# Kernel tuning notes

Measured on AMD Instinct MI355X. Metric: run time of the kernel, lower is better.

Reference implementation:

```python
import jax, jax.numpy as jnp
import numpy as np
from jax import lax

B, T, C = 2, 2048, 2048
N_HEADS, N_KV_HEADS = 16, 1
HEAD_DIM = C // N_HEADS  # 128
ROPE_THETA = 10000.0


def setup_inputs() -> dict:
    key = jax.random.key(0)
    ks = jax.random.split(key, 8)
    x = jax.random.normal(ks[0], (B, T, C), dtype=jnp.float32)
    # rotary frequencies: freqs_cis = exp(1j * t * theta^{-2i/d}) -> cos/sin halves
    inv_freq = 1.0 / (ROPE_THETA ** (np.arange(0, HEAD_DIM, 2, dtype=np.float32) / HEAD_DIM))
    t = np.arange(T, dtype=np.float32)
    ang = np.outer(t, inv_freq)  # [T, HEAD_DIM//2]
    freqs_cos = jnp.asarray(np.cos(ang), dtype=jnp.float32)
    freqs_sin = jnp.asarray(np.sin(ang), dtype=jnp.float32)
    # additive causal mask [1,1,T,T]
    causal = jnp.tril(jnp.ones((T, T), dtype=bool))
    mask = jnp.where(causal, 0.0, -1e9).astype(jnp.float32)[None, None]
    s = 0.02
    wq_k = jax.random.normal(ks[1], (C, N_HEADS * HEAD_DIM), dtype=jnp.float32) * s
    wk_k = jax.random.normal(ks[2], (C, N_KV_HEADS * HEAD_DIM), dtype=jnp.float32) * s
    wv_k = jax.random.normal(ks[3], (C, N_KV_HEADS * HEAD_DIM), dtype=jnp.float32) * s
    wo_k = jax.random.normal(ks[4], (N_HEADS * HEAD_DIM, C), dtype=jnp.float32) * s
    return {
        "x": x, "freqs_cos": freqs_cos, "freqs_sin": freqs_sin, "mask": mask,
        "wq_k": wq_k, "wq_b": jnp.zeros((N_HEADS * HEAD_DIM,), jnp.float32),
        "wk_k": wk_k, "wk_b": jnp.zeros((N_KV_HEADS * HEAD_DIM,), jnp.float32),
        "wv_k": wv_k, "wv_b": jnp.zeros((N_KV_HEADS * HEAD_DIM,), jnp.float32),
        "wo_k": wo_k, "wo_b": jnp.zeros((C,), jnp.float32),
    }


def _rope(xq, xk, cos, sin):
    # xq: [B,T,H,D], xk: [B,T,Hkv,D]; cos/sin: [T, D//2]
    def rot(v):
        vr = v.reshape(*v.shape[:-1], -1, 2)  # [..., D//2, 2]
        re, im = vr[..., 0], vr[..., 1]
        c = cos[None, :, None, :]
        s = sin[None, :, None, :]
        out_re = re * c - im * s
        out_im = re * s + im * c
        return jnp.stack([out_re, out_im], axis=-1).reshape(v.shape)
    return rot(xq), rot(xk)


def reference(x, freqs_cos, freqs_sin, mask, wq_k, wq_b, wk_k, wk_b, wv_k, wv_b, wo_k, wo_b):
    b, t, c = x.shape
    head_dim = c // N_HEADS
    q = (x @ wq_k + wq_b).reshape(b, t, N_HEADS, head_dim)
    k = (x @ wk_k + wk_b).reshape(b, t, N_KV_HEADS, head_dim)
    v = (x @ wv_k + wv_b).reshape(b, t, N_KV_HEADS, head_dim)
    q, k = _rope(q, k, freqs_cos[:t], freqs_sin[:t])
    if N_HEADS > N_KV_HEADS:
        rep = N_HEADS // N_KV_HEADS
        k = jnp.repeat(k, rep, axis=2)
        v = jnp.repeat(v, rep, axis=2)
    q, k, v = (jnp.swapaxes(a, 1, 2) for a in (q, k, v))  # [B,H,T,D]
    scale = 1.0 / jnp.sqrt(jnp.asarray(head_dim, x.dtype))
    scores = jnp.einsum('bhid,bhjd->bhij', q, k) * scale + mask
    scores = scores - lax.stop_gradient(jnp.max(scores, axis=-1, keepdims=True))
    w = jnp.exp(scores)
    attn = w / jnp.sum(w, axis=-1, keepdims=True)
    out = jnp.einsum('bhij,bhjd->bhid', attn, v)
    out = jnp.swapaxes(out, 1, 2).reshape(b, t, -1)
    return out @ wo_k + wo_b
```

## Files before the change

### kernel.cpp

```cpp
#include <hip/hip_runtime.h>
#include <hip/hip_bf16.h>

typedef __bf16 bf16;
typedef __bf16 bf16x4 __attribute__((ext_vector_type(4)));
typedef __bf16 bf16x8 __attribute__((ext_vector_type(8)));
typedef float  f32x4  __attribute__((ext_vector_type(4)));

#define MFMA(a,b,c) __builtin_amdgcn_mfma_f32_16x16x32_bf16(a,b,c,0,0,0)

__device__ __forceinline__ void load_lds16(const void* gptr, void* lptr) {
  __builtin_amdgcn_global_load_lds(
      (const __attribute__((address_space(1))) void*)gptr,
      (__attribute__((address_space(3))) void*)lptr, 16, 0, 0);
}


__global__ void cvt_bf16(const float* __restrict__ in, bf16* __restrict__ out, int n4) {
  int i = blockIdx.x * blockDim.x + threadIdx.x;
  if (i >= n4) return;
  float4 v = ((const float4*)in)[i];
  bf16x4 o = { (bf16)v.x, (bf16)v.y, (bf16)v.z, (bf16)v.w };
  ((bf16x4*)out)[i] = o;
}

__global__ void transpose_w(const float* __restrict__ src, bf16* __restrict__ dst, int ncols) {
  __shared__ float tl[32][33];
  int n0 = blockIdx.x * 32, k0 = blockIdx.y * 32;
  int tx = threadIdx.x, ty = threadIdx.y;
  for (int i = 0; i < 4; ++i)
    tl[ty + i*8][tx] = src[(size_t)(k0 + ty + i*8) * ncols + n0 + tx];
  __syncthreads();
  for (int i = 0; i < 4; ++i)
    dst[(size_t)(n0 + ty + i*8) * 2048 + k0 + tx] = (bf16)tl[tx][ty + i*8];
}

__global__ void concat_bias(const float* __restrict__ qb, const float* __restrict__ kb,
                            const float* __restrict__ vb, float* __restrict__ o) {
  int i = blockIdx.x * 256 + threadIdx.x;
  if (i >= 2304) return;
  o[i] = (i < 2048) ? qb[i] : (i < 2176 ? kb[i - 2048] : vb[i - 2176]);
}


template<bool OUT_F32>
__global__ __launch_bounds__(256) void gemm_bt(
    const bf16* __restrict__ A, const bf16* __restrict__ Bt,
    void* __restrict__ Cout, const float* __restrict__ bias,
    int M, int N, int K)
{
  __shared__ char smem[32768];
  char* As = smem;
  char* Bs = smem + 16384;
  const int tid = threadIdx.x;
  const int w = tid >> 6, l = tid & 63;
  const int lg = l >> 4, ll = l & 15;
  const int n0 = blockIdx.x * 128, m0 = blockIdx.y * 128;
  const int wr = w >> 1, wc = w & 1;

  f32x4 acc[4][4];
  for (int i = 0; i < 4; ++i) for (int j = 0; j < 4; ++j) acc[i][j] = (f32x4){0.f,0.f,0.f,0.f};

  for (int k0 = 0; k0 < K; k0 += 64) {
    for (int t = 0; t < 4; ++t) {
      int seg = w*4 + t;
      int row = seg*8 + (l >> 3);
      int cb  = (l & 7) * 8;
      load_lds16(A  + (size_t)(m0 + row) * K + k0 + cb, As + seg*1024);
      load_lds16(Bt + (size_t)(n0 + row) * K + k0 + cb, Bs + seg*1024);
    }
    __syncthreads();
    for (int kc = 0; kc < 2; ++kc) {
      bf16x8 af[4], bfr[4];
      for (int ai = 0; ai < 4; ++ai)
        af[ai]  = *(const bf16x8*)(As + (wr*64 + ai*16 + ll)*128 + kc*64 + lg*16);
      for (int bj = 0; bj < 4; ++bj)
        bfr[bj] = *(const bf16x8*)(Bs + (wc*64 + bj*16 + ll)*128 + kc*64 + lg*16);
      for (int ai = 0; ai < 4; ++ai)
        for (int bj = 0; bj < 4; ++bj)
          acc[ai][bj] = MFMA(af[ai], bfr[bj], acc[ai][bj]);
    }
    __syncthreads();
  }

  for (int ai = 0; ai < 4; ++ai) {
    int row = m0 + wr*64 + ai*16 + lg*4;
    for (int bj = 0; bj < 4; ++bj) {
      int col = n0 + wc*64 + bj*16 + ll;
      float bv = bias[col];
      for (int r = 0; r < 4; ++r) {
        float v = acc[ai][bj][r] + bv;
        if constexpr (OUT_F32) ((float*)Cout)[(size_t)(row + r) * N + col] = v;
        else                   ((bf16*)Cout)[(size_t)(row + r) * N + col] = (bf16)v;
      }
    }
  }
}


__global__ void rope_q(bf16* __restrict__ qkv, const float* __restrict__ fc, const float* __restrict__ fs) {
  int idx = blockIdx.x * 256 + threadIdx.x;
  int d = idx & 63, h = (idx >> 6) & 15, bt = idx >> 10;
  int t = bt & 2047;
  bf16* p = qkv + (size_t)bt * 2304 + h * 128 + 2 * d;
  float re = (float)p[0], im = (float)p[1];
  float c = fc[t*64 + d], s = fs[t*64 + d];
  p[0] = (bf16)(re * c - im * s);
  p[1] = (bf16)(re * s + im * c);
}

__global__ void rope_k(bf16* __restrict__ qkv, const float* __restrict__ fc, const float* __restrict__ fs) {
  int idx = blockIdx.x * 256 + threadIdx.x;
  int d = idx & 63, bt = idx >> 6;
  int t = bt & 2047;
  bf16* p = qkv + (size_t)bt * 2304 + 2048 + 2 * d;
  float re = (float)p[0], im = (float)p[1];
  float c = fc[t*64 + d], s = fs[t*64 + d];
  p[0] = (bf16)(re * c - im * s);
  p[1] = (bf16)(re * s + im * c);
}

__global__ void transpose_v(const bf16* __restrict__ qkv, bf16* __restrict__ vt) {
  __shared__ bf16 tl[32][33];
  int t0 = blockIdx.x * 32, d0 = blockIdx.y * 32, b = blockIdx.z;
  int tx = threadIdx.x, ty = threadIdx.y;
  for (int i = 0; i < 4; ++i)
    tl[ty + i*8][tx] = qkv[(size_t)(b*2048 + t0 + ty + i*8) * 2304 + 2176 + d0 + tx];
  __syncthreads();
  for (int i = 0; i < 4; ++i)
    vt[(size_t)(b*128 + d0 + ty + i*8) * 2048 + t0 + tx] = tl[tx][ty + i*8];
}


__global__ __launch_bounds__(256) void attn_kernel(
    const bf16* __restrict__ qkv, const bf16* __restrict__ vt, bf16* __restrict__ aout)
{
  constexpr int T = 2048, NQKV = 2304, D = 128;
  const int tid = threadIdx.x;
  const int w = tid >> 6, l = tid & 63;
  const int lg = l >> 4, ll = l & 15;
  const int h  = blockIdx.y;
  const int b  = blockIdx.z;

  __shared__ char smem[16384 + 16384 + 8192];
  char* Ks = smem;
  char* Vs = smem + 16384;
  char* Ps = smem + 32768 + w*2048;

  const size_t qkvb = (size_t)b * T * NQKV;
  const float scale = 0.08838834764831845f;

  for (int half = 0; half < 2; ++half) {
    const int x  = half ? (31 - blockIdx.x) : blockIdx.x;
    const int q0 = x * 64;

    bf16x8 qf[4];
    {
      int row = q0 + w*16 + ll;
      const bf16* qrow = qkv + qkvb + (size_t)row * NQKV + h * D;
      for (int kc = 0; kc < 4; ++kc)
        qf[kc] = *(const bf16x8*)(qrow + kc*32 + lg*8);
    }

    f32x4 acc[8];
    for (int dt = 0; dt < 8; ++dt) acc[dt] = (f32x4){0.f,0.f,0.f,0.f};
    float mx[4], sm[4];
    for (int r = 0; r < 4; ++r) { mx[r] = -3e38f; sm[r] = 0.f; }

    for (int j0 = 0; j0 <= q0; j0 += 64) {
      for (int t = 0; t < 4; ++t) {
        int seg = w*4 + t;
        int row = seg*4 + (l >> 4);
        int gcol = (((l & 15) * 16) ^ ((row & 7) << 4)) >> 1;
        load_lds16(qkv + qkvb + (size_t)(j0 + row) * NQKV + 2048 + gcol, Ks + seg*1024);
      }
      for (int t = 0; t < 4; ++t) {
        int seg = w*4 + t;
        int row = seg*8 + (l >> 3);
        int gcol = (((l & 7) * 16) ^ ((row & 7) << 4)) >> 1;
        load_lds16(vt + (size_t)(b*D + row) * T + j0 + gcol, Vs + seg*1024);
      }
      __syncthreads();

      f32x4 sv[4];
      for (int jt = 0; jt < 4; ++jt) {
        int row = jt*16 + ll;
        f32x4 s = (f32x4){0.f,0.f,0.f,0.f};
        for (int kc = 0; kc < 4; ++kc) {
          bf16x8 kf = *(const bf16x8*)(Ks + row*256 + ((kc*64 + lg*16) ^ ((row & 7) << 4)));
          s = MFMA(qf[kc], kf, s);
        }
        sv[jt] = s;
      }

      if (j0 == q0) {
        for (int jt = 0; jt < 4; ++jt)
          for (int r = 0; r < 4; ++r) {
            int i = w*16 + lg*4 + r;
            int j = jt*16 + ll;
            float v = sv[jt][r] * scale;
            sv[jt][r] = (j <= i) ? v : -1e9f;
          }
      } else {
        for (int jt = 0; jt < 4; ++jt)
          for (int r = 0; r < 4; ++r)
            sv[jt][r] *= scale;
      }

      for (int r = 0; r < 4; ++r) {
        float tm = fmaxf(fmaxf(sv[0][r], sv[1][r]), fmaxf(sv[2][r], sv[3][r]));
        tm = fmaxf(tm, __shfl_xor(tm, 1));
        tm = fmaxf(tm, __shfl_xor(tm, 2));
        tm = fmaxf(tm, __shfl_xor(tm, 4));
        tm = fmaxf(tm, __shfl_xor(tm, 8));
        float mo = mx[r];
        float mn = fmaxf(mo, tm);
        mx[r] = mn;
        float fac = __expf(mo - mn);
        float ps = 0.f;
        for (int jt = 0; jt < 4; ++jt) {
          float p = __expf(sv[jt][r] - mn);
          sv[jt][r] = p;
          ps += p;
        }
        ps += __shfl_xor(ps, 1);
        ps += __shfl_xor(ps, 2);
        ps += __shfl_xor(ps, 4);
        ps += __shfl_xor(ps, 8);
        sm[r] = sm[r] * fac + ps;
        for (int dt = 0; dt < 8; ++dt) acc[dt][r] *= fac;
      }

      for (int jt = 0; jt < 4; ++jt)
        for (int r = 0; r < 4; ++r) {
          int prow = lg*4 + r;
          *(bf16*)(Ps + prow*128 + (((jt*16 + ll)*2) ^ ((prow & 7) << 4))) = (bf16)sv[jt][r];
        }
      asm volatile("s_waitcnt lgkmcnt(0)" ::: "memory");

      bf16x8 pa[2];
      for (int c = 0; c < 2; ++c)
        pa[c] = *(const bf16x8*)(Ps + ll*128 + ((c*64 + lg*16) ^ ((ll & 7) << 4)));
      for (int dt = 0; dt < 8; ++dt) {
        int row = dt*16 + ll;
        for (int c = 0; c < 2; ++c) {
          bf16x8 vf = *(const bf16x8*)(Vs + row*128 + ((c*64 + lg*16) ^ ((row & 7) << 4)));
          acc[dt] = MFMA(pa[c], vf, acc[dt]);
        }
      }
      __syncthreads();
    }

    for (int dt = 0; dt < 8; ++dt) {
      int col = h*D + dt*16 + ll;
      for (int r = 0; r < 4; ++r) {
        int row = q0 + w*16 + lg*4 + r;
        float v = acc[dt][r] / sm[r];
        aout[(size_t)(b*T + row) * 2048 + col] = (bf16)v;
      }
    }
  }
}


extern "C" void kernel_launch(void* const* d_in, const int* in_sizes, int n_in,
                              void* d_out, int out_size, void* d_ws, size_t ws_size,
                              hipStream_t stream) {
  const float* x  = (const float*)d_in[0];
  const float* fc = (const float*)d_in[1];
  const float* fs = (const float*)d_in[2];
  const float* wq = (const float*)d_in[4];
  const float* qb = (const float*)d_in[5];
  const float* wk = (const float*)d_in[6];
  const float* kb = (const float*)d_in[7];
  const float* wv = (const float*)d_in[8];
  const float* vb = (const float*)d_in[9];
  const float* wo = (const float*)d_in[10];
  const float* ob = (const float*)d_in[11];

  char* ws = (char*)d_ws;
  bf16*  x_bf   = (bf16*)(ws);
  bf16*  qkv    = (bf16*)(ws + 16777216);
  bf16*  wqkv_t = (bf16*)(ws + 35651584);
  bf16*  wo_t   = (bf16*)(ws + 45088768);
  bf16*  v_t    = (bf16*)(ws + 53477376);
  float* qkvb   = (float*)(ws + 54525952);
  bf16*  a_out  = x_bf;

  cvt_bf16<<<8192, 256, 0, stream>>>(x, x_bf, 2097152);
  transpose_w<<<dim3(64,64), dim3(32,8), 0, stream>>>(wq, wqkv_t, 2048);
  transpose_w<<<dim3(4,64),  dim3(32,8), 0, stream>>>(wk, wqkv_t + (size_t)2048*2048, 128);
  transpose_w<<<dim3(4,64),  dim3(32,8), 0, stream>>>(wv, wqkv_t + (size_t)2176*2048, 128);
  transpose_w<<<dim3(64,64), dim3(32,8), 0, stream>>>(wo, wo_t, 2048);
  concat_bias<<<9, 256, 0, stream>>>(qb, kb, vb, qkvb);

  gemm_bt<false><<<dim3(18,32), 256, 0, stream>>>(x_bf, wqkv_t, qkv, qkvb, 4096, 2304, 2048);

  rope_q<<<16384, 256, 0, stream>>>(qkv, fc, fs);
  rope_k<<<1024, 256, 0, stream>>>(qkv, fc, fs);
  transpose_v<<<dim3(64,4,2), dim3(32,8), 0, stream>>>(qkv, v_t);

  attn_kernel<<<dim3(16,16,2), 256, 0, stream>>>(qkv, v_t, a_out);

  gemm_bt<true><<<dim3(16,32), 256, 0, stream>>>(a_out, wo_t, d_out, ob, 4096, 2048, 2048);
}
```

Baseline: 378.6 us.

## Double attention KV tile to 128, lazy softmax rescale, XCD-swizzle GEMM blocks

Attention now processes 128 keys per iteration with 64KB LDS, aliasing the P buffer onto the K tile after an added barrier, halving loop iterations and barriers. Softmax rescaling of the accumulator is skipped unless the running max grows by more than 8, reducing exp and multiply work. MFMA sections are wrapped in s_setprio, and the GEMM remaps workgroup ids so neighboring tiles share an XCD for cache reuse. The larger LDS footprint lowers occupancy and the causal diagonal now wastes more masked work.

Measured after the change: 430.1 us. +13.6%, slower.

```diff
diff --git a/kernel.cpp b/kernel.cpp
--- a/kernel.cpp
+++ b/kernel.cpp
@@ -54,7 +54,12 @@
   const int tid = threadIdx.x;
   const int w = tid >> 6, l = tid & 63;
   const int lg = l >> 4, ll = l & 15;
-  const int n0 = blockIdx.x * 128, m0 = blockIdx.y * 128;
+
+  const int nwg = gridDim.x * gridDim.y;
+  int wg = blockIdx.y * gridDim.x + blockIdx.x;
+  wg = (wg & 7) * (nwg >> 3) + (wg >> 3);
+  const int n0 = (wg % gridDim.x) * 128;
+  const int m0 = (wg / gridDim.x) * 128;
   const int wr = w >> 1, wc = w & 1;
 
   f32x4 acc[4][4];
@@ -141,10 +146,10 @@
   const int h  = blockIdx.y;
   const int b  = blockIdx.z;
 
-  __shared__ char smem[16384 + 16384 + 8192];
+  __shared__ char smem[65536];
   char* Ks = smem;
-  char* Vs = smem + 16384;
-  char* Ps = smem + 32768 + w*2048;
+  char* Vs = smem + 32768;
+  char* Ps = smem + w*8192;
 
   const size_t qkvb = (size_t)b * T * NQKV;
   const float scale = 0.08838834764831845f;
@@ -166,23 +171,24 @@
     float mx[4], sm[4];
     for (int r = 0; r < 4; ++r) { mx[r] = -3e38f; sm[r] = 0.f; }
 
-    for (int j0 = 0; j0 <= q0; j0 += 64) {
-      for (int t = 0; t < 4; ++t) {
-        int seg = w*4 + t;
+    for (int j0 = 0; j0 <= q0; j0 += 128) {
+      for (int t = 0; t < 8; ++t) {
+        int seg = w*8 + t;
         int row = seg*4 + (l >> 4);
-        int gcol = (((l & 15) * 16) ^ ((row & 7) << 4)) >> 1;
-        load_lds16(qkv + qkvb + (size_t)(j0 + row) * NQKV + 2048 + gcol, Ks + seg*1024);
-      }
-      for (int t = 0; t < 4; ++t) {
-        int seg = w*4 + t;
-        int row = seg*8 + (l >> 3);
-        int gcol = (((l & 7) * 16) ^ ((row & 7) << 4)) >> 1;
-        load_lds16(vt + (size_t)(b*D + row) * T + j0 + gcol, Vs + seg*1024);
+        int gb  = ((l & 15) * 16) ^ ((row & 7) << 4);
+        load_lds16(qkv + qkvb + (size_t)(j0 + row) * NQKV + 2048 + (gb >> 1), Ks + seg*1024);
+      }
+      for (int t = 0; t < 8; ++t) {
+        int seg = w*8 + t;
+        int row = seg*4 + (l >> 4);
+        int gb  = ((l & 15) * 16) ^ ((row & 7) << 4);
+        load_lds16(vt + (size_t)(b*D + row) * T + j0 + (gb >> 1), Vs + seg*1024);
       }
       __syncthreads();
 
-      f32x4 sv[4];
-      for (int jt = 0; jt < 4; ++jt) {
+      f32x4 sv[8];
+      __builtin_amdgcn_s_setprio(1);
+      for (int jt = 0; jt < 8; ++jt) {
         int row = jt*16 + ll;
         f32x4 s = (f32x4){0.f,0.f,0.f,0.f};
         for (int kc = 0; kc < 4; ++kc) {
@@ -191,34 +197,43 @@
         }
         sv[jt] = s;
       }
-
-      if (j0 == q0) {
-        for (int jt = 0; jt < 4; ++jt)
+      __builtin_amdgcn_s_setprio(0);
+
+      __syncthreads();
+
+      if (j0 + 127 > q0) {
+        int i_g = q0 + w*16 + lg*4;
+        for (int jt = 0; jt < 8; ++jt) {
+          int j_g = j0 + jt*16 + ll;
           for (int r = 0; r < 4; ++r) {
-            int i = w*16 + lg*4 + r;
-            int j = jt*16 + ll;
             float v = sv[jt][r] * scale;
-            sv[jt][r] = (j <= i) ? v : -1e9f;
+            sv[jt][r] = (j_g <= i_g + r) ? v : -1e9f;
           }
+        }
       } else {
-        for (int jt = 0; jt < 4; ++jt)
+        for (int jt = 0; jt < 8; ++jt)
           for (int r = 0; r < 4; ++r)
             sv[jt][r] *= scale;
       }
 
       for (int r = 0; r < 4; ++r) {
-        float tm = fmaxf(fmaxf(sv[0][r], sv[1][r]), fmaxf(sv[2][r], sv[3][r]));
+        float tm = -3e38f;
+        for (int jt = 0; jt < 8; ++jt) tm = fmaxf(tm, sv[jt][r]);
         tm = fmaxf(tm, __shfl_xor(tm, 1));
         tm = fmaxf(tm, __shfl_xor(tm, 2));
         tm = fmaxf(tm, __shfl_xor(tm, 4));
         tm = fmaxf(tm, __shfl_xor(tm, 8));
         float mo = mx[r];
-        float mn = fmaxf(mo, tm);
-        mx[r] = mn;
-        float fac = __expf(mo - mn);
+        if (!__all(tm - mo <= 8.f)) {
+          float mn = fmaxf(mo, tm);
+          float fac = __expf(mo - mn);
+          mx[r] = mn; sm[r] *= fac;
+          for (int dt = 0; dt < 8; ++dt) acc[dt][r] *= fac;
+          mo = mn;
+        }
         float ps = 0.f;
-        for (int jt = 0; jt < 4; ++jt) {
-          float p = __expf(sv[jt][r] - mn);
+        for (int jt = 0; jt < 8; ++jt) {
+          float p = __expf(sv[jt][r] - mo);
           sv[jt][r] = p;
           ps += p;
         }
@@ -226,27 +241,28 @@
         ps += __shfl_xor(ps, 2);
         ps += __shfl_xor(ps, 4);
         ps += __shfl_xor(ps, 8);
-        sm[r] = sm[r] * fac + ps;
-        for (int dt = 0; dt < 8; ++dt) acc[dt][r] *= fac;
-      }
-
-      for (int jt = 0; jt < 4; ++jt)
+        sm[r] += ps;
+      }
+
+      for (int jt = 0; jt < 8; ++jt)
         for (int r = 0; r < 4; ++r) {
           int prow = lg*4 + r;
-          *(bf16*)(Ps + prow*128 + (((jt*16 + ll)*2) ^ ((prow & 7) << 4))) = (bf16)sv[jt][r];
+          *(bf16*)(Ps + prow*256 + (((jt*16 + ll)*2) ^ ((prow & 7) << 4))) = (bf16)sv[jt][r];
         }
       asm volatile("s_waitcnt lgkmcnt(0)" ::: "memory");
 
-      bf16x8 pa[2];
-      for (int c = 0; c < 2; ++c)
-        pa[c] = *(const bf16x8*)(Ps + ll*128 + ((c*64 + lg*16) ^ ((ll & 7) << 4)));
+      bf16x8 pa[4];
+      for (int c = 0; c < 4; ++c)
+        pa[c] = *(const bf16x8*)(Ps + ll*256 + ((c*64 + lg*16) ^ ((ll & 7) << 4)));
+      __builtin_amdgcn_s_setprio(1);
       for (int dt = 0; dt < 8; ++dt) {
         int row = dt*16 + ll;
-        for (int c = 0; c < 2; ++c) {
-          bf16x8 vf = *(const bf16x8*)(Vs + row*128 + ((c*64 + lg*16) ^ ((row & 7) << 4)));
+        for (int c = 0; c < 4; ++c) {
+          bf16x8 vf = *(const bf16x8*)(Vs + row*256 + ((c*64 + lg*16) ^ ((row & 7) << 4)));
           acc[dt] = MFMA(pa[c], vf, acc[dt]);
         }
       }
+      __builtin_amdgcn_s_setprio(0);
       __syncthreads();
     }
 
```

## Use 256x256 double-buffered swizzled GEMM tiles with 512-thread blocks

Applied to the files above, without the earlier changes.

Replaces the 128x128 single-buffered GEMM with a 256x256-tile kernel of 8 waves. It double-buffers LDS stages using vmcnt waits, XOR-swizzles LDS rows to avoid bank conflicts, and remaps block IDs to improve L2 locality. The aim is more reuse per byte loaded and overlap of global loads with MFMA work. The cost is far fewer blocks (144 and 128) than the CU count, so much of the GPU may sit idle, and the 128KB LDS footprint limits occupancy.

Measured after the change: 361.1 us. 4.6% less time.

```diff
diff --git a/kernel.cpp b/kernel.cpp
--- a/kernel.cpp
+++ b/kernel.cpp
@@ -43,49 +43,74 @@
 
 
 template<bool OUT_F32>
-__global__ __launch_bounds__(256) void gemm_bt(
+__global__ __launch_bounds__(512) void gemm_bt256(
     const bf16* __restrict__ A, const bf16* __restrict__ Bt,
     void* __restrict__ Cout, const float* __restrict__ bias,
     int M, int N, int K)
 {
-  __shared__ char smem[32768];
-  char* As = smem;
-  char* Bs = smem + 16384;
+  __shared__ char smem[131072];
   const int tid = threadIdx.x;
   const int w = tid >> 6, l = tid & 63;
   const int lg = l >> 4, ll = l & 15;
-  const int n0 = blockIdx.x * 128, m0 = blockIdx.y * 128;
-  const int wr = w >> 1, wc = w & 1;
-
-  f32x4 acc[4][4];
-  for (int i = 0; i < 4; ++i) for (int j = 0; j < 4; ++j) acc[i][j] = (f32x4){0.f,0.f,0.f,0.f};
-
-  for (int k0 = 0; k0 < K; k0 += 64) {
+  const int wm = w >> 2, wn = w & 3;
+
+  const int nwg = gridDim.x * gridDim.y;
+  int bid = blockIdx.y * gridDim.x + blockIdx.x;
+  int work = (bid & 7) * (nwg >> 3) + (bid >> 3);
+  const int n0 = (work % gridDim.x) * 256;
+  const int m0 = (work / gridDim.x) * 256;
+
+  const int nt = K >> 6;
+
+  f32x4 acc[8][4];
+  for (int i = 0; i < 8; ++i) for (int j = 0; j < 4; ++j) acc[i][j] = (f32x4){0.f,0.f,0.f,0.f};
+
+  auto STAGE = [&](int buf, int kt) {
+    char* As = smem + buf * 65536;
+    char* Bs = As + 32768;
+    int k0 = kt * 64;
     for (int t = 0; t < 4; ++t) {
-      int seg = w*4 + t;
-      int row = seg*8 + (l >> 3);
-      int cb  = (l & 7) * 8;
-      load_lds16(A  + (size_t)(m0 + row) * K + k0 + cb, As + seg*1024);
-      load_lds16(Bt + (size_t)(n0 + row) * K + k0 + cb, Bs + seg*1024);
-    }
-    __syncthreads();
+      int seg = w * 4 + t;
+      int row = seg * 8 + (l >> 3);
+      int cb  = ((l & 7) * 16) ^ ((row & 7) << 4);
+      load_lds16(A  + (size_t)(m0 + row) * K + k0 + (cb >> 1), As + seg * 1024);
+      load_lds16(Bt + (size_t)(n0 + row) * K + k0 + (cb >> 1), Bs + seg * 1024);
+    }
+  };
+
+  STAGE(0, 0);
+
+  for (int kt = 0; kt < nt; ++kt) {
+    if (kt + 1 < nt) {
+      STAGE((kt + 1) & 1, kt + 1);
+      asm volatile("s_waitcnt vmcnt(8)" ::: "memory");
+    } else {
+      asm volatile("s_waitcnt vmcnt(0)" ::: "memory");
+    }
+    __builtin_amdgcn_s_barrier();
+    const char* As = smem + (kt & 1) * 65536;
+    const char* Bs = As + 32768;
     for (int kc = 0; kc < 2; ++kc) {
-      bf16x8 af[4], bfr[4];
-      for (int ai = 0; ai < 4; ++ai)
-        af[ai]  = *(const bf16x8*)(As + (wr*64 + ai*16 + ll)*128 + kc*64 + lg*16);
-      for (int bj = 0; bj < 4; ++bj)
-        bfr[bj] = *(const bf16x8*)(Bs + (wc*64 + bj*16 + ll)*128 + kc*64 + lg*16);
-      for (int ai = 0; ai < 4; ++ai)
+      bf16x8 af[8], bfr[4];
+      for (int ai = 0; ai < 8; ++ai) {
+        int row = wm * 128 + ai * 16 + ll;
+        af[ai] = *(const bf16x8*)(As + row * 128 + ((kc * 64 + lg * 16) ^ ((row & 7) << 4)));
+      }
+      for (int bj = 0; bj < 4; ++bj) {
+        int row = wn * 64 + bj * 16 + ll;
+        bfr[bj] = *(const bf16x8*)(Bs + row * 128 + ((kc * 64 + lg * 16) ^ ((row & 7) << 4)));
+      }
+      for (int ai = 0; ai < 8; ++ai)
         for (int bj = 0; bj < 4; ++bj)
           acc[ai][bj] = MFMA(af[ai], bfr[bj], acc[ai][bj]);
     }
-    __syncthreads();
+    __builtin_amdgcn_s_barrier();
   }
 
-  for (int ai = 0; ai < 4; ++ai) {
-    int row = m0 + wr*64 + ai*16 + lg*4;
+  for (int ai = 0; ai < 8; ++ai) {
+    int row = m0 + wm * 128 + ai * 16 + lg * 4;
     for (int bj = 0; bj < 4; ++bj) {
-      int col = n0 + wc*64 + bj*16 + ll;
+      int col = n0 + wn * 64 + bj * 16 + ll;
       float bv = bias[col];
       for (int r = 0; r < 4; ++r) {
         float v = acc[ai][bj][r] + bv;
@@ -293,7 +318,7 @@
   transpose_w<<<dim3(64,64), dim3(32,8), 0, stream>>>(wo, wo_t, 2048);
   concat_bias<<<9, 256, 0, stream>>>(qb, kb, vb, qkvb);
 
-  gemm_bt<false><<<dim3(18,32), 256, 0, stream>>>(x_bf, wqkv_t, qkv, qkvb, 4096, 2304, 2048);
+  gemm_bt256<false><<<dim3(9,16), 512, 0, stream>>>(x_bf, wqkv_t, qkv, qkvb, 4096, 2304, 2048);
 
   rope_q<<<16384, 256, 0, stream>>>(qkv, fc, fs);
   rope_k<<<1024, 256, 0, stream>>>(qkv, fc, fs);
@@ -301,5 +326,5 @@
 
   attn_kernel<<<dim3(16,16,2), 256, 0, stream>>>(qkv, v_t, a_out);
 
-  gemm_bt<true><<<dim3(16,32), 256, 0, stream>>>(a_out, wo_t, d_out, ob, 4096, 2048, 2048);
-}
+  gemm_bt256<true><<<dim3(8,16), 512, 0, stream>>>(a_out, wo_t, d_out, ob, 4096, 2048, 2048);
+}
```
